# Performance work log

Hardware: AMD Instinct MI355X
Metric: run time of the kernel (lower is better)

The kernel has to match this reference:

```python
import jax, jax.numpy as jnp
import numpy as np

B, S, H, C, LAT = 16, 16, 501, 10, 56
G = H + S  # gate/map input width (mod=None)


def _linear(x, w, b):
    # torch nn.Linear convention: w is [out, in]
    return x @ w.T + b


def _gru_cell(x, h, w_ih, w_hh, b_ih, b_hh):
    gi = _linear(x, w_ih, b_ih)
    gh = _linear(h, w_hh, b_hh)
    i_r, i_z, i_n = jnp.split(gi, 3, axis=-1)
    h_r, h_z, h_n = jnp.split(gh, 3, axis=-1)
    r = jax.nn.sigmoid(i_r + h_r)
    u = jax.nn.sigmoid(i_z + h_z)
    n = jnp.tanh(i_n + r * h_n)
    return (1.0 - u) * n + u * h


def setup_inputs() -> dict:
    key = jax.random.key(0)
    ks = jax.random.split(key, 16)
    w = lambda k, shape: jax.random.normal(k, shape, dtype=jnp.float32) * 0.05
    return {
        "z": jax.random.normal(ks[0], (B, LAT), dtype=jnp.float32),
        "dep_graph": jax.random.uniform(ks[1], (B, S, S), dtype=jnp.float32),
        "node_encoding": jax.random.normal(ks[2], (B, S, C), dtype=jnp.float32),
        "lin1_w": w(ks[3], (H, LAT)), "lin1_b": jnp.zeros((H,), jnp.float32),
        "av1_w": w(ks[4], (2 * H, H)), "av1_b": jnp.zeros((2 * H,), jnp.float32),
        "av2_w": w(ks[5], (C, 2 * H)), "av2_b": jnp.zeros((C,), jnp.float32),
        "ae1_w": w(ks[6], (4 * H, 2 * H)), "ae1_b": jnp.zeros((4 * H,), jnp.float32),
        "ae2_w": w(ks[7], (1, 4 * H)), "ae2_b": jnp.zeros((1,), jnp.float32),
        "gate_w": w(ks[8], (H, G)), "gate_b": jnp.zeros((H,), jnp.float32),
        "map_w": w(ks[9], (H, G)), "map_b": jnp.zeros((H,), jnp.float32),
        "gru_w_ih": w(ks[10], (3 * H, C)), "gru_b_ih": jnp.zeros((3 * H,), jnp.float32),
        "gru_w_hh": w(ks[11], (3 * H, H)), "gru_b_hh": jnp.zeros((3 * H,), jnp.float32),
    }


def reference(z, dep_graph, node_encoding, lin1_w, lin1_b, av1_w, av1_b, av2_w, av2_b,
              ae1_w, ae1_b, ae2_w, ae2_b, gate_w, gate_b, map_w, map_b,
              gru_w_ih, gru_b_ih, gru_w_hh, gru_b_hh):
    Bv, Sv, _ = dep_graph.shape
    Hv = lin1_w.shape[0]
    dt = dep_graph.dtype
    # 'ordering' one-hot positional features, identical per batch element
    ordering = jnp.broadcast_to(jnp.eye(Sv, dtype=dt), (Bv, Sv, Sv))
    col = jnp.arange(Sv)

    add_vertex = lambda x: _linear(jax.nn.relu(_linear(x, av1_w, av1_b)), av2_w, av2_b)
    add_edge = lambda x: _linear(jax.nn.relu(_linear(x, ae1_w, ae1_b)), ae2_w, ae2_b)
    gru = lambda x, h: _gru_cell(x, h, gru_w_ih, gru_w_hh, gru_b_ih, gru_b_hh)

    graph_state = _linear(z, lin1_w, lin1_b)                     # [B, H]
    nhs = jnp.zeros((Bv, Sv, Hv), dt)                            # node hidden states
    gen_dep = jnp.zeros_like(dep_graph)
    gen_nodes = []

    for index in range(Sv):  # static outer loop (seq_len is small & fixed)
        gen_nodes.append(add_vertex(graph_state))                # logits [B, C]
        x_t = node_encoding[:, index]                            # [B, C]
        h0 = graph_state if index == 0 else jnp.zeros((Bv, Hv), dt)
        hv = gru(x_t, h0)
        if index > 0:
            ancestors = dep_graph[:, index]                      # [B, S]

            def inner(carry, v_j):
                hv, nhs = carry
                hidden_j = jnp.take(nhs, v_j, axis=1)            # [B, H]
                edge = add_edge(jnp.concatenate([hv, hidden_j], axis=1))[:, 0]  # [B]
                am = ancestors * (col >= v_j).astype(dt)         # masked ancestors [B, S]
                mhs = jnp.concatenate([nhs, ordering], axis=-1) * am[:, :, None]  # [B,S,H+S]
                h_in = jnp.sum(
                    jax.nn.sigmoid(_linear(mhs, gate_w, gate_b))
                    * _linear(mhs, map_w, map_b)
                    * am[:, :, None],
                    axis=1,
                )                                                # [B, H]
                hv_new = gru(x_t, h_in)
                nhs = nhs.at[:, index].set(hv_new)
                return (hv_new, nhs), edge

            (hv, nhs), edges = jax.lax.scan(inner, (hv, nhs), jnp.arange(index - 1, -1, -1))
            # edges[k] corresponds to v_j = index-1-k -> flip to ascending v_j order
            gen_dep = gen_dep.at[:, index, :index].set(jnp.flip(edges, 0).T)
        nhs = nhs.at[:, index].set(hv)
        graph_state = hv

    gen_node_encoding = jnp.stack(gen_nodes, axis=1)             # [B, S, C]
    return gen_dep, gen_node_encoding
```

## Files before the change

kernel.cpp:

```cpp
#include <hip/hip_runtime.h>

#define DEVFN static __device__ __forceinline__

namespace {
constexpr int Hc = 501, Gc = 517;
constexpr size_t OFF_WGP = 0;
constexpr size_t OFF_WMP = OFF_WGP + (size_t)512 * 512;
constexpr size_t OFF_WHP = OFF_WMP + (size_t)512 * 512;
constexpr size_t OFF_WHV = OFF_WHP + (size_t)512 * 1536;
constexpr size_t OFF_WHJ = OFF_WHV + (size_t)2048 * 512;
constexpr size_t OFF_WAV = OFF_WHJ + (size_t)2048 * 512;
constexpr size_t OFF_GCOL= OFF_WAV + (size_t)1024 * 512;
constexpr size_t OFF_MCOL= OFF_GCOL + (size_t)512 * 16;
constexpr size_t OFF_GI  = OFF_MCOL + (size_t)512 * 16;
constexpr size_t OFF_GS0 = OFF_GI  + (size_t)16 * 16 * 1536;
constexpr size_t OFF_HSEQ= OFF_GS0 + (size_t)16 * 512;
constexpr size_t OFF_HINS= OFF_HSEQ+ (size_t)16 * 136 * 512;
constexpr size_t OFF_TBUF= OFF_HINS+ (size_t)120 * 16 * 512;
constexpr size_t WS_FLOATS=OFF_TBUF+ (size_t)16 * 16 * 1024;
constexpr size_t N_FLG   = (size_t)8 * 256 * 32;
constexpr size_t WS_NEED = (WS_FLOATS + N_FLG + 512 + 64) * 4;

constexpr int SM_WHH = 0;
constexpr int SM_ST  = 24576;
constexpr int SM_QM  = 25600;
constexpr int SM_PS  = 26560;
constexpr int SM_GC  = 27072;
constexpr int SM_GIL = 27584;
constexpr int SM_BHH = 27680;
constexpr int SM_GB  = 27728;
constexpr int SM_MB  = 27744;
constexpr int SM_DEP = 27760;
constexpr int SM_TOT = 27792;
constexpr int F_BHJ = 8192;
constexpr int F_RED = 10112;
constexpr int F_TOT = 10376;
}

DEVFN float sigf(float x)  { return 1.0f / (1.0f + __expf(-x)); }
DEVFN float tanhf_(float x){ float e2 = __expf(2.0f * x); return 1.0f - 2.0f / (e2 + 1.0f); }
DEVFN void  stgf(float* p, float v) { __hip_atomic_store(p, v, __ATOMIC_RELAXED, __HIP_MEMORY_SCOPE_AGENT); }
DEVFN size_t hslotf(int b, int slot) { return OFF_HSEQ + ((size_t)b * 136 + slot) * 512; }
DEVFN int trif(int idx) { return idx * (idx + 1) / 2; }

struct KArgs {
  const float* in[21];
  float* out;
  float* wsf;
};

DEVFN float4 maskpad(float4 v, int k4) {
  if (k4 == 125) { v.y = 0.f; v.z = 0.f; v.w = 0.f; }
  else if (k4 > 125) { v.x = v.y = v.z = v.w = 0.f; }
  return v;
}

__global__ __launch_bounds__(256) void k0_init(KArgs a) {
  const float* z    = a.in[0];  const float* enc  = a.in[2];
  const float* lin1w= a.in[3];  const float* lin1b= a.in[4];
  const float* gatew= a.in[13]; const float* mapw = a.in[15];
  const float* wih  = a.in[17]; const float* bih  = a.in[18];
  const float* whh  = a.in[19];
  float* wsf = a.wsf;
  const int gtid = blockIdx.x * 256 + threadIdx.x;
  const int NTH = 256 * 256;

  for (size_t t = gtid; t < (size_t)512 * 512; t += NTH) {
    int i = t >> 9, k = t & 511;
    bool ok = (i < Hc && k < Hc);
    wsf[OFF_WGP + t] = ok ? gatew[(size_t)i * Gc + k] : 0.f;
    wsf[OFF_WMP + t] = ok ? mapw [(size_t)i * Gc + k] : 0.f;
  }
  for (size_t t = gtid; t < (size_t)512 * 1536; t += NTH) {
    int i = t / 1536, rk = t % 1536, r = rk >> 9, k = rk & 511;
    wsf[OFF_WHP + t] = (i < Hc && k < Hc) ? whh[((size_t)r * Hc + i) * Hc + k] : 0.f;
  }
  for (size_t t = gtid; t < (size_t)512 * 16; t += NTH) {
    int i = t >> 4, j = t & 15;
    wsf[OFF_GCOL + t] = (i < Hc) ? gatew[(size_t)i * Gc + Hc + j] : 0.f;
    wsf[OFF_MCOL + t] = (i < Hc) ? mapw [(size_t)i * Gc + Hc + j] : 0.f;
  }
  for (size_t t = gtid; t < (size_t)16 * 16 * 1503; t += NTH) {
    int r = t % 1503; size_t bi = t / 1503;
    float acc = bih[r];
    const float* x = enc + bi * 10;
    const float* w = wih + (size_t)r * 10;
    #pragma unroll
    for (int c = 0; c < 10; ++c) acc = fmaf(w[c], x[c], acc);
    wsf[OFF_GI + bi * 1536 + r] = acc;
  }
  for (size_t t = gtid; t < (size_t)16 * 512; t += NTH) {
    int b = t >> 9, i = t & 511;
    float v = 0.f;
    if (i < Hc) {
      float acc = lin1b[i];
      const float* zz = z + (size_t)b * 56;
      const float* w  = lin1w + (size_t)i * 56;
      for (int k = 0; k < 56; ++k) acc = fmaf(w[k], zz[k], acc);
      v = acc;
    }
    wsf[OFF_GS0 + t] = v;
  }
  for (size_t t = gtid; t < 4096; t += NTH) a.out[t] = 0.f;
  unsigned* FLG = (unsigned*)a.wsf + WS_FLOATS;
  for (size_t t = gtid; t < N_FLG + 512; t += NTH) FLG[t] = 0u;
}

__global__ __launch_bounds__(256, 1) void k1_scan(KArgs a) {
  const int blk = blockIdx.x, tid = threadIdx.x;
  const int g = blk >> 5, m = blk & 31;
  const int ig = tid >> 4, l = tid & 15;
  const int i = m * 16 + ig;
  float* wsf = a.wsf;
  unsigned* FLG = (unsigned*)a.wsf + WS_FLOATS;
  const float* dep  = a.in[1];
  const float* gateb= a.in[14]; const float* mapb = a.in[16];
  const float* bhh  = a.in[20];

  __shared__ float smem[SM_TOT];
  int pid = 0;

  {
    float4* d = (float4*)smem;
    const float4* s = ((const float4*)(wsf + OFF_WHP)) + (size_t)m * 6144;
    for (int t = tid; t < 6144; t += 256) d[t] = s[t];
    for (int t = tid; t < 512; t += 256) {
      int q = t >> 8, r2 = t & 255, ii = r2 >> 4, j = r2 & 15;
      smem[SM_GC + t] = wsf[(q ? OFF_MCOL : OFF_GCOL) + (size_t)(m * 16 + ii) * 16 + j];
    }
    if (tid < 16) {
      int iG = m * 16 + tid;
      smem[SM_GB + tid] = (iG < Hc) ? gateb[iG] : 0.f;
      smem[SM_MB + tid] = (iG < Hc) ? mapb[iG]  : 0.f;
    }
    if (tid < 48) {
      int r = tid >> 4, ii = tid & 15, iG = m * 16 + ii;
      smem[SM_BHH + tid] = (iG < Hc) ? bhh[r * Hc + iG] : 0.f;
    }
  }
  float4 wgr[8], wmr[8];
  {
    const float4* pg = ((const float4*)(wsf + OFF_WGP)) + (size_t)i * 128;
    const float4* pm = ((const float4*)(wsf + OFF_WMP)) + (size_t)i * 128;
    #pragma unroll
    for (int t = 0; t < 8; ++t) { wgr[t] = pg[t * 16 + l]; wmr[t] = pm[t * 16 + l]; }
  }
  __syncthreads();

  auto flagbar = [&]() {
    __syncthreads();
    if (tid == 0)
      __hip_atomic_store(FLG + ((size_t)g * 256 + pid) * 32 + m, (unsigned)(pid + 1),
                         __ATOMIC_RELAXED, __HIP_MEMORY_SCOPE_AGENT);
    if (tid < 32) {
      unsigned* p = FLG + ((size_t)g * 256 + pid) * 32 + tid;
      while (__hip_atomic_load(p, __ATOMIC_RELAXED, __HIP_MEMORY_SCOPE_AGENT) != (unsigned)(pid + 1))
        __builtin_amdgcn_s_sleep(2);
    }
    __syncthreads();
    ++pid;
  };

  auto stage2v = [&](size_t o0, size_t o1) {
    float4* d = (float4*)(smem + SM_ST);
    if (tid < 128) d[tid] = ((const float4*)(wsf + o0))[tid];
    else           d[tid] = ((const float4*)(wsf + o1))[tid - 128];
  };
  auto stagegi = [&](int index) {
    if (tid >= 64 && tid < 160) {
      int t = tid - 64, b = t / 48, r = (t / 16) % 3, ii = t & 15, iG = m * 16 + ii;
      smem[SM_GIL + (b * 3 + r) * 16 + ii] =
        (iG < Hc) ? wsf[OFF_GI + ((size_t)(2 * g + b) * 16 + index) * 1536 + (size_t)r * Hc + iG] : 0.f;
    }
  };
  auto s1core = [&](float& aq0, float& am0, float& aq1, float& am1) {
    const float4* h0 = (const float4*)(smem + SM_ST);
    const float4* h1 = (const float4*)(smem + SM_ST + 512);
    float q0 = 0.f, m0 = 0.f, q1 = 0.f, m1 = 0.f;
    #pragma unroll
    for (int t = 0; t < 8; ++t) {
      int k4 = t * 16 + l;
      float4 a0 = h0[k4], a1 = h1[k4];
      q0 = fmaf(wgr[t].x, a0.x, q0); q0 = fmaf(wgr[t].y, a0.y, q0);
      q0 = fmaf(wgr[t].z, a0.z, q0); q0 = fmaf(wgr[t].w, a0.w, q0);
      m0 = fmaf(wmr[t].x, a0.x, m0); m0 = fmaf(wmr[t].y, a0.y, m0);
      m0 = fmaf(wmr[t].z, a0.z, m0); m0 = fmaf(wmr[t].w, a0.w, m0);
      q1 = fmaf(wgr[t].x, a1.x, q1); q1 = fmaf(wgr[t].y, a1.y, q1);
      q1 = fmaf(wgr[t].z, a1.z, q1); q1 = fmaf(wgr[t].w, a1.w, q1);
      m1 = fmaf(wmr[t].x, a1.x, m1); m1 = fmaf(wmr[t].y, a1.y, m1);
      m1 = fmaf(wmr[t].z, a1.z, m1); m1 = fmaf(wmr[t].w, a1.w, m1);
    }
    q0 += __shfl_xor(q0, 1); q0 += __shfl_xor(q0, 2); q0 += __shfl_xor(q0, 4); q0 += __shfl_xor(q0, 8);
    m0 += __shfl_xor(m0, 1); m0 += __shfl_xor(m0, 2); m0 += __shfl_xor(m0, 4); m0 += __shfl_xor(m0, 8);
    q1 += __shfl_xor(q1, 1); q1 += __shfl_xor(q1, 2); q1 += __shfl_xor(q1, 4); q1 += __shfl_xor(q1, 8);
    m1 += __shfl_xor(m1, 1); m1 += __shfl_xor(m1, 2); m1 += __shfl_xor(m1, 4); m1 += __shfl_xor(m1, 8);
    aq0 = q0; am0 = m0; aq1 = q1; am1 = m1;
  };
  auto s2core = [&](int dstSlot) {
    const float4* W  = ((const float4*)smem) + ig * 384;
    const float4* h0 = (const float4*)(smem + SM_ST);
    const float4* h1 = (const float4*)(smem + SM_ST + 512);
    float gr0 = 0.f, gz0 = 0.f, gn0 = 0.f, gr1 = 0.f, gz1 = 0.f, gn1 = 0.f;
    #pragma unroll
    for (int t = 0; t < 8; ++t) {
      int k4 = t * 16 + l;
      float4 hv0 = h0[k4], hv1 = h1[k4];
      float4 a0 = W[k4], a1 = W[128 + k4], a2 = W[256 + k4];
      gr0 = fmaf(a0.x, hv0.x, gr0); gr0 = fmaf(a0.y, hv0.y, gr0); gr0 = fmaf(a0.z, hv0.z, gr0); gr0 = fmaf(a0.w, hv0.w, gr0);
      gz0 = fmaf(a1.x, hv0.x, gz0); gz0 = fmaf(a1.y, hv0.y, gz0); gz0 = fmaf(a1.z, hv0.z, gz0); gz0 = fmaf(a1.w, hv0.w, gz0);
      gn0 = fmaf(a2.x, hv0.x, gn0); gn0 = fmaf(a2.y, hv0.y, gn0); gn0 = fmaf(a2.z, hv0.z, gn0); gn0 = fmaf(a2.w, hv0.w, gn0);
      gr1 = fmaf(a0.x, hv1.x, gr1); gr1 = fmaf(a0.y, hv1.y, gr1); gr1 = fmaf(a0.z, hv1.z, gr1); gr1 = fmaf(a0.w, hv1.w, gr1);
      gz1 = fmaf(a1.x, hv1.x, gz1); gz1 = fmaf(a1.y, hv1.y, gz1); gz1 = fmaf(a1.z, hv1.z, gz1); gz1 = fmaf(a1.w, hv1.w, gz1);
      gn1 = fmaf(a2.x, hv1.x, gn1); gn1 = fmaf(a2.y, hv1.y, gn1); gn1 = fmaf(a2.z, hv1.z, gn1); gn1 = fmaf(a2.w, hv1.w, gn1);
    }
    gr0 += __shfl_xor(gr0, 1); gr0 += __shfl_xor(gr0, 2); gr0 += __shfl_xor(gr0, 4); gr0 += __shfl_xor(gr0, 8);
    gz0 += __shfl_xor(gz0, 1); gz0 += __shfl_xor(gz0, 2); gz0 += __shfl_xor(gz0, 4); gz0 += __shfl_xor(gz0, 8);
    gn0 += __shfl_xor(gn0, 1); gn0 += __shfl_xor(gn0, 2); gn0 += __shfl_xor(gn0, 4); gn0 += __shfl_xor(gn0, 8);
    gr1 += __shfl_xor(gr1, 1); gr1 += __shfl_xor(gr1, 2); gr1 += __shfl_xor(gr1, 4); gr1 += __shfl_xor(gr1, 8);
    gz1 += __shfl_xor(gz1, 1); gz1 += __shfl_xor(gz1, 2); gz1 += __shfl_xor(gz1, 4); gz1 += __shfl_xor(gz1, 8);
    gn1 += __shfl_xor(gn1, 1); gn1 += __shfl_xor(gn1, 2); gn1 += __shfl_xor(gn1, 4); gn1 += __shfl_xor(gn1, 8);
    if (l < 2) {
      int b = l;
      float gr = l ? gr1 : gr0, gz = l ? gz1 : gz0, gn = l ? gn1 : gn0;
      float h  = smem[SM_ST + b * 512 + i];
      float rr = sigf(smem[SM_GIL + (b * 3 + 0) * 16 + ig] + gr + smem[SM_BHH + 0 + ig]);
      float uu = sigf(smem[SM_GIL + (b * 3 + 1) * 16 + ig] + gz + smem[SM_BHH + 16 + ig]);
      float nn = tanhf_(smem[SM_GIL + (b * 3 + 2) * 16 + ig] + rr * (gn + smem[SM_BHH + 32 + ig]));
      float v = (1.f - uu) * nn + uu * h;
      if (i >= Hc) v = 0.f;
      stgf(wsf + hslotf(2 * g + b, dstSlot) + i, v);
    }
  };

  stage2v(OFF_GS0 + (size_t)(2 * g) * 512, OFF_GS0 + (size_t)(2 * g + 1) * 512);
  stagegi(0);
  __syncthreads();
  s2core(0);
  flagbar();

  for (int index = 1; index < 16; ++index) {
    stage2v(hslotf(2 * g,     trif(index - 1) + index - 1),
            hslotf(2 * g + 1, trif(index - 1) + index - 1));
    if (tid < 32) {
      int b = tid >> 4, j = tid & 15;
      smem[SM_DEP + b * 16 + j] = dep[((size_t)(2 * g + b) * 16 + index) * 16 + j];
    }
    stagegi(index);
    __syncthreads();
    {
      float aq0, am0, aq1, am1;
      s1core(aq0, am0, aq1, am1);
      if (l < 2) {
        float aq = l ? aq1 : aq0, am = l ? am1 : am0;
        smem[SM_QM + ((l * 2 + 0) * 15 + (index - 1)) * 16 + ig] = aq + smem[SM_GC + ig * 16 + (index - 1)];
        smem[SM_QM + ((l * 2 + 1) * 15 + (index - 1)) * 16 + ig] = am + smem[SM_GC + 256 + ig * 16 + (index - 1)];
      }
    }
    __syncthreads();
    if (l < 2) {
      float acc = 0.f, gb = smem[SM_GB + ig], mb = smem[SM_MB + ig];
      for (int j = 15; j >= 0; --j) {
        if (j != index) {
          float aa = smem[SM_DEP + l * 16 + j];
          float q, mm;
          if (j < index) { q = smem[SM_QM + ((l * 2 + 0) * 15 + j) * 16 + ig];
                           mm = smem[SM_QM + ((l * 2 + 1) * 15 + j) * 16 + ig]; }
          else           { q = smem[SM_GC + ig * 16 + j];
                           mm = smem[SM_GC + 256 + ig * 16 + j]; }
          float sg = sigf(fmaf(aa, q, gb));
          acc = fmaf(aa * sg, fmaf(aa, mm, mb), acc);
        }
        smem[SM_PS + (l * 16 + ig) * 16 + j] = acc;
      }
    } else if (l < 4) {
      int b = l - 2;
      float rr = sigf(smem[SM_GIL + (b * 3 + 0) * 16 + ig] + smem[SM_BHH + 0 + ig]);
      float uu = sigf(smem[SM_GIL + (b * 3 + 1) * 16 + ig] + smem[SM_BHH + 16 + ig]);
      float nn = tanhf_(smem[SM_GIL + (b * 3 + 2) * 16 + ig] + rr * smem[SM_BHH + 32 + ig]);
      float v = (1.f - uu) * nn;
      if (i >= Hc) v = 0.f;
      stgf(wsf + hslotf(2 * g + b, trif(index) + 0) + i, v);
    }
    __syncthreads();
    if (l < 2) {
      int b = l;
      float gb = smem[SM_GB + ig], mb = smem[SM_MB + ig];
      float aI = smem[SM_DEP + b * 16 + index];
      float Qi = smem[SM_GC + ig * 16 + index], Mi = smem[SM_GC + 256 + ig * 16 + index];
      float f = aI * sigf(fmaf(aI, Qi, gb)) * fmaf(aI, Mi, mb);
      float v = smem[SM_PS + (b * 16 + ig) * 16 + (index - 1)] + f;
      if (i >= Hc) v = 0.f;
      stgf(wsf + OFF_HINS + ((size_t)(index * (index - 1) / 2 + 0) * 16 + (2 * g + b)) * 512 + i, v);
    }
    flagbar();

    for (int s = 0; s < index; ++s) {
      stage2v(OFF_HINS + ((size_t)(index * (index - 1) / 2 + s) * 16 + (2 * g + 0)) * 512,
              OFF_HINS + ((size_t)(index * (index - 1) / 2 + s) * 16 + (2 * g + 1)) * 512);
      __syncthreads();
      s2core(trif(index) + s + 1);
      flagbar();
      if (s + 1 < index) {
        int ss = s + 1, vj = index - 1 - ss;
        stage2v(hslotf(2 * g, trif(index) + ss), hslotf(2 * g + 1, trif(index) + ss));
        __syncthreads();
        {
          float aq0, am0, aq1, am1;
          s1core(aq0, am0, aq1, am1);
          if (l < 2) {
            int b = l;
            float aq = l ? aq1 : aq0, am = l ? am1 : am0;
            float gb = smem[SM_GB + ig], mb = smem[SM_MB + ig];
            float aI = smem[SM_DEP + b * 16 + index];
            float Qi = aq + smem[SM_GC + ig * 16 + index];
            float Mi = am + smem[SM_GC + 256 + ig * 16 + index];
            float f = aI * sigf(fmaf(aI, Qi, gb)) * fmaf(aI, Mi, mb);
            float v = smem[SM_PS + (b * 16 + ig) * 16 + vj] + f;
            if (i >= Hc) v = 0.f;
            stgf(wsf + OFF_HINS + ((size_t)(index * (index - 1) / 2 + ss) * 16 + (2 * g + b)) * 512 + i, v);
          }
        }
        flagbar();
      }
    }
  }
}

__global__ __launch_bounds__(256, 1) void k2_fin(KArgs a) {
  const int blk = blockIdx.x, tid = threadIdx.x;
  float* wsf = a.wsf;
  unsigned* FLG = (unsigned*)a.wsf + WS_FLOATS;
  unsigned* F1F = FLG + N_FLG;
  const float* ae1w = a.in[9];
  const float* av1w = a.in[5];

  __shared__ float smem[F_TOT];
  const int b = blk >> 4, rs = blk & 15;
  const int il = tid >> 3, l8 = tid & 7;
  float4* lds4 = (float4*)smem;

  for (int t = tid; t < 2048; t += 256) {
    int j = t >> 7, k4 = t & 127;
    float4 v = {0.f, 0.f, 0.f, 0.f};
    if (j < 15) v = maskpad(((const float4*)(wsf + hslotf(b, trif(j) + j)))[k4], k4);
    lds4[t] = v;
  }
  __syncthreads();
  {
    const int rbase = rs * 126 + il * 4;
    for (int half = 0; half < 2; ++half) {
      int jbase = half * 8;
      float acc[4][8];
      #pragma unroll
      for (int q = 0; q < 4; ++q)
        #pragma unroll
        for (int j = 0; j < 8; ++j) acc[q][j] = 0.f;
      for (int s = 0; s < 63; ++s) {
        int k = s * 8 + l8;
        if (k < 501) {
          float w[4];
          #pragma unroll
          for (int q = 0; q < 4; ++q)
            w[q] = (rbase + q < 2004) ? ae1w[(size_t)(rbase + q) * 1002 + 501 + k] : 0.f;
          float hv[8];
          #pragma unroll
          for (int j = 0; j < 8; ++j) hv[j] = smem[(jbase + j) * 512 + k];
          #pragma unroll
          for (int q = 0; q < 4; ++q)
            #pragma unroll
            for (int j = 0; j < 8; ++j) acc[q][j] = fmaf(w[q], hv[j], acc[q][j]);
        }
      }
      #pragma unroll
      for (int q = 0; q < 4; ++q) {
        bool rowok = (il * 4 + q < 126) && (rbase + q < 2004);
        #pragma unroll
        for (int j = 0; j < 8; ++j) {
          float v = acc[q][j];
          v += __shfl_xor(v, 1); v += __shfl_xor(v, 2); v += __shfl_xor(v, 4);
          if (l8 == 0 && rowok && (jbase + j) < 15)
            smem[F_BHJ + (jbase + j) * 128 + il * 4 + q] = v;
        }
      }
    }
  }
  __syncthreads();
  for (int t = tid; t < 2048; t += 256) {
    int idx = t >> 7, k4 = t & 127;
    const float4* src = (idx == 0)
      ? ((const float4*)(wsf + OFF_GS0 + (size_t)b * 512))
      : ((const float4*)(wsf + hslotf(b, trif(idx - 1) + idx - 1)));
    lds4[t] = maskpad(src[k4], k4);
  }
  __syncthreads();
  {
    const float* av1b = a.in[6];
    const int rbase = rs * 63 + il * 2;
    for (int half = 0; half < 2; ++half) {
      int jbase = half * 8;
      float acc[2][8];
      #pragma unroll
      for (int q = 0; q < 2; ++q)
        #pragma unroll
        for (int j = 0; j < 8; ++j) acc[q][j] = 0.f;
      for (int s = 0; s < 63; ++s) {
        int k = s * 8 + l8;
        if (k < 501) {
          float w[2];
          #pragma unroll
          for (int q = 0; q < 2; ++q)
            w[q] = (rbase + q < 1002) ? av1w[(size_t)(rbase + q) * 501 + k] : 0.f;
          float hv[8];
          #pragma unroll
          for (int j = 0; j < 8; ++j) hv[j] = smem[(jbase + j) * 512 + k];
          #pragma unroll
          for (int q = 0; q < 2; ++q)
            #pragma unroll
            for (int j = 0; j < 8; ++j) acc[q][j] = fmaf(w[q], hv[j], acc[q][j]);
        }
      }
      #pragma unroll
      for (int q = 0; q < 2; ++q) {
        int r = rbase + q;
        bool rowok = (il * 2 + q < 63) && (r < 1002);
        float b1 = rowok ? av1b[r] : 0.f;
        #pragma unroll
        for (int j = 0; j < 8; ++j) {
          float v = acc[q][j];
          v += __shfl_xor(v, 1); v += __shfl_xor(v, 2); v += __shfl_xor(v, 4);
          if (l8 == 0 && rowok)
            stgf(wsf + OFF_TBUF + ((size_t)b * 16 + jbase + j) * 1024 + r, fmaxf(v + b1, 0.f));
        }
      }
    }
  }
  __syncthreads();
  if (tid == 0)
    __hip_atomic_store(F1F + b * 16 + rs, 1u, __ATOMIC_RELAXED, __HIP_MEMORY_SCOPE_AGENT);

  const float* ae1b = a.in[10]; const float* ae2w = a.in[11]; const float* ae2b = a.in[12];
  const int rbase = rs * 126 + il * 4;
  for (int chunk = 0; chunk < 15; ++chunk) {
    int idxs[8], vjs[8]; bool tval[8];
    #pragma unroll
    for (int j = 0; j < 8; ++j) {
      int e = chunk * 8 + j;
      if (e < 120) {
        int ix = 1, rem = e;
        while (rem >= ix) { rem -= ix; ++ix; }
        idxs[j] = ix; vjs[j] = rem; tval[j] = true;
      } else { idxs[j] = 1; vjs[j] = 0; tval[j] = false; }
    }
    __syncthreads();
    for (int t = tid; t < 1024; t += 256) {
      int sl = t >> 7, k4 = t & 127;
      int sE = idxs[sl] - 1 - vjs[sl];
      lds4[t] = maskpad(((const float4*)(wsf + hslotf(b, trif(idxs[sl]) + sE)))[k4], k4);
    }
    __syncthreads();
    float part[8];
    #pragma unroll
    for (int j = 0; j < 8; ++j) part[j] = 0.f;
    float acc[4][8];
    #pragma unroll
    for (int q = 0; q < 4; ++q)
      #pragma unroll
      for (int j = 0; j < 8; ++j) acc[q][j] = 0.f;
    for (int s = 0; s < 63; ++s) {
      int k = s * 8 + l8;
      if (k < 501) {
        float w[4];
        #pragma unroll
        for (int q = 0; q < 4; ++q)
          w[q] = (rbase + q < 2004) ? ae1w[(size_t)(rbase + q) * 1002 + k] : 0.f;
        float hv[8];
        #pragma unroll
        for (int j = 0; j < 8; ++j) hv[j] = smem[j * 512 + k];
        #pragma unroll
        for (int q = 0; q < 4; ++q)
          #pragma unroll
          for (int j = 0; j < 8; ++j) acc[q][j] = fmaf(w[q], hv[j], acc[q][j]);
      }
    }
    #pragma unroll
    for (int q = 0; q < 4; ++q) {
      int r = rbase + q;
      bool rowok = (il * 4 + q < 126) && (r < 2004);
      float aer = rowok ? ae2w[r] : 0.f;
      float b1r = rowok ? ae1b[r] : 0.f;
      #pragma unroll
      for (int j = 0; j < 8; ++j) {
        float v = acc[q][j];
        v += __shfl_xor(v, 1); v += __shfl_xor(v, 2); v += __shfl_xor(v, 4);
        if (l8 == 0 && rowok && tval[j]) {
          float bh = smem[F_BHJ + vjs[j] * 128 + il * 4 + q];
          part[j] = fmaf(aer, fmaxf(v + bh + b1r, 0.f), part[j]);
        }
      }
    }
    if (l8 == 0) {
      #pragma unroll
      for (int j = 0; j < 8; ++j) smem[F_RED + il * 8 + j] = part[j];
    }
    __syncthreads();
    if (tid < 8) {
      float v = 0.f;
      for (int q = 0; q < 32; ++q) v += smem[F_RED + q * 8 + tid];
      if (rs == 0) v += ae2b[0];
      if (tval[tid])
        atomicAdd(a.out + ((size_t)b * 16 + idxs[tid]) * 16 + vjs[tid], v);
    }
    __syncthreads();
  }
  if (tid < 16) {
    unsigned* p = F1F + b * 16 + tid;
    while (__hip_atomic_load(p, __ATOMIC_RELAXED, __HIP_MEMORY_SCOPE_AGENT) != 1u)
      __builtin_amdgcn_s_sleep(2);
  }
  __syncthreads();
  {
    const float* av2w = a.in[7]; const float* av2b = a.in[8];
    const float* tb = wsf + OFF_TBUF + ((size_t)b * 16 + rs) * 1024;
    float accn[10];
    #pragma unroll
    for (int c = 0; c < 10; ++c) accn[c] = 0.f;
    for (int r = tid; r < 1002; r += 256) {
      float tv = tb[r];
      #pragma unroll
      for (int c = 0; c < 10; ++c) accn[c] = fmaf(av2w[(size_t)c * 1002 + r], tv, accn[c]);
    }
    #pragma unroll
    for (int c = 0; c < 10; ++c) {
      float v = accn[c];
      for (int m2 = 1; m2 < 64; m2 <<= 1) v += __shfl_xor(v, m2);
      if ((tid & 63) == 0) smem[F_RED + (tid >> 6) * 10 + c] = v;
    }
    __syncthreads();
    if (tid == 0) {
      for (int c = 0; c < 10; ++c) {
        float v = av2b[c] + smem[F_RED + c] + smem[F_RED + 10 + c] + smem[F_RED + 20 + c] + smem[F_RED + 30 + c];
        stgf(a.out + 4096 + ((size_t)b * 16 + rs) * 10 + c, v);
      }
    }
  }
}

extern "C" void kernel_launch(void* const* d_in, const int* in_sizes, int n_in,
                              void* d_out, int out_size, void* d_ws, size_t ws_size,
                              hipStream_t stream) {
  (void)in_sizes; (void)n_in; (void)out_size;
  if (ws_size < WS_NEED) return;
  KArgs a;
  for (int k = 0; k < 21; ++k) a.in[k] = (const float*)d_in[k];
  a.out = (float*)d_out;
  a.wsf = (float*)d_ws;
  k0_init<<<256, 256, 0, stream>>>(a);
  k1_scan<<<256, 256, 0, stream>>>(a);
  k2_fin <<<256, 256, 0, stream>>>(a);
}
```

Measured before the change: 1.330 ms.

## Replace flag barriers with NaN-sentinel data polling in scan kernel

Removes the per-step cross-block flag barrier and instead pre-fills the hidden-state and h_in buffers with NaN sentinels. Each block polls the specific data it needs until the values are no longer NaN, turning the global barrier into fine-grained dataflow synchronization. This cuts the barrier round trips and lets blocks proceed as soon as their inputs arrive. The risks are correctness: it relies on non-NaN data, on write visibility without acquire ordering, and on float4 pieces not being torn. It also adds init work to fill the buffers.

```diff
diff --git a/kernel.cpp b/kernel.cpp
--- a/kernel.cpp
+++ b/kernel.cpp
@@ -101,9 +101,14 @@
     }
     wsf[OFF_GS0 + t] = v;
   }
+  {
+    unsigned* p = (unsigned*)(wsf + OFF_HSEQ);
+    const size_t n = OFF_TBUF - OFF_HSEQ;
+    for (size_t t = gtid; t < n; t += NTH) p[t] = 0x7FC00000u;
+  }
   for (size_t t = gtid; t < 4096; t += NTH) a.out[t] = 0.f;
   unsigned* FLG = (unsigned*)a.wsf + WS_FLOATS;
-  for (size_t t = gtid; t < N_FLG + 512; t += NTH) FLG[t] = 0u;
+  for (size_t t = gtid; t < 512; t += NTH) FLG[N_FLG + t] = 0u;
 }
 
 __global__ __launch_bounds__(256, 1) void k1_scan(KArgs a) {
@@ -112,13 +117,11 @@
   const int ig = tid >> 4, l = tid & 15;
   const int i = m * 16 + ig;
   float* wsf = a.wsf;
-  unsigned* FLG = (unsigned*)a.wsf + WS_FLOATS;
   const float* dep  = a.in[1];
   const float* gateb= a.in[14]; const float* mapb = a.in[16];
   const float* bhh  = a.in[20];
 
   __shared__ float smem[SM_TOT];
-  int pid = 0;
 
   {
     float4* d = (float4*)smem;
@@ -145,26 +148,19 @@
     #pragma unroll
     for (int t = 0; t < 8; ++t) { wgr[t] = pg[t * 16 + l]; wmr[t] = pm[t * 16 + l]; }
   }
-  __syncthreads();
-
-  auto flagbar = [&]() {
-    __syncthreads();
-    if (tid == 0)
-      __hip_atomic_store(FLG + ((size_t)g * 256 + pid) * 32 + m, (unsigned)(pid + 1),
-                         __ATOMIC_RELAXED, __HIP_MEMORY_SCOPE_AGENT);
-    if (tid < 32) {
-      unsigned* p = FLG + ((size_t)g * 256 + pid) * 32 + tid;
-      while (__hip_atomic_load(p, __ATOMIC_RELAXED, __HIP_MEMORY_SCOPE_AGENT) != (unsigned)(pid + 1))
-        __builtin_amdgcn_s_sleep(2);
-    }
-    __syncthreads();
-    ++pid;
-  };
-
-  auto stage2v = [&](size_t o0, size_t o1) {
-    float4* d = (float4*)(smem + SM_ST);
-    if (tid < 128) d[tid] = ((const float4*)(wsf + o0))[tid];
-    else           d[tid] = ((const float4*)(wsf + o1))[tid - 128];
+
+  auto pollst = [&](size_t o0, size_t o1) {
+    size_t base = (tid < 128) ? o0 : o1;
+    int idx = (tid & 127) * 4;
+    const volatile float* s = (const volatile float*)(wsf + base) + idx;
+    float x, y, zv, w;
+    for (;;) {
+      x = s[0]; y = s[1]; zv = s[2]; w = s[3];
+      if (!(x != x || y != y || zv != zv || w != w)) break;
+      __builtin_amdgcn_s_sleep(1);
+    }
+    float* d = smem + SM_ST + (tid < 128 ? 0 : 512) + idx;
+    d[0] = x; d[1] = y; d[2] = zv; d[3] = w;
   };
   auto stagegi = [&](int index) {
     if (tid >= 64 && tid < 160) {
@@ -232,15 +228,16 @@
     }
   };
 
-  stage2v(OFF_GS0 + (size_t)(2 * g) * 512, OFF_GS0 + (size_t)(2 * g + 1) * 512);
+  __syncthreads();
+  pollst(OFF_GS0 + (size_t)(2 * g) * 512, OFF_GS0 + (size_t)(2 * g + 1) * 512);
   stagegi(0);
   __syncthreads();
   s2core(0);
-  flagbar();
 
   for (int index = 1; index < 16; ++index) {
-    stage2v(hslotf(2 * g,     trif(index - 1) + index - 1),
-            hslotf(2 * g + 1, trif(index - 1) + index - 1));
+    __syncthreads();
+    pollst(hslotf(2 * g,     trif(index - 1) + index - 1),
+           hslotf(2 * g + 1, trif(index - 1) + index - 1));
     if (tid < 32) {
       int b = tid >> 4, j = tid & 15;
       smem[SM_DEP + b * 16 + j] = dep[((size_t)(2 * g + b) * 16 + index) * 16 + j];
@@ -292,17 +289,17 @@
       if (i >= Hc) v = 0.f;
       stgf(wsf + OFF_HINS + ((size_t)(index * (index - 1) / 2 + 0) * 16 + (2 * g + b)) * 512 + i, v);
     }
-    flagbar();
 
     for (int s = 0; s < index; ++s) {
-      stage2v(OFF_HINS + ((size_t)(index * (index - 1) / 2 + s) * 16 + (2 * g + 0)) * 512,
-              OFF_HINS + ((size_t)(index * (index - 1) / 2 + s) * 16 + (2 * g + 1)) * 512);
+      __syncthreads();
+      pollst(OFF_HINS + ((size_t)(index * (index - 1) / 2 + s) * 16 + (2 * g + 0)) * 512,
+             OFF_HINS + ((size_t)(index * (index - 1) / 2 + s) * 16 + (2 * g + 1)) * 512);
       __syncthreads();
       s2core(trif(index) + s + 1);
-      flagbar();
       if (s + 1 < index) {
         int ss = s + 1, vj = index - 1 - ss;
-        stage2v(hslotf(2 * g, trif(index) + ss), hslotf(2 * g + 1, trif(index) + ss));
+        __syncthreads();
+        pollst(hslotf(2 * g, trif(index) + ss), hslotf(2 * g + 1, trif(index) + ss));
         __syncthreads();
         {
           float aq0, am0, aq1, am1;
@@ -320,7 +317,6 @@
             stgf(wsf + OFF_HINS + ((size_t)(index * (index - 1) / 2 + ss) * 16 + (2 * g + b)) * 512 + i, v);
           }
         }
-        flagbar();
       }
     }
   }
```

After: 1.370 ms. 1.03x slower.

## Move weight repacking and GI precompute into scan kernel; prefetch edge-MLP inputs

Applied to the files above, without the earlier changes.

The scan kernel now reads gate, map and GRU weights straight from the raw inputs into shared memory and registers, and computes the input-gate projections and initial state locally. This removes the large repack pass in the init kernel and its workspace round-trip, and the init kernel shrinks to 64 blocks. The final kernel register-prefetches the next chunk of hidden states into a double-buffered LDS region and prefetches the av1 input tile. Bounds checks in its inner loops are replaced by clamped indices. Strided non-vectorised weight loads in the scan kernel's prologue may cost more per block.

```diff
diff --git a/kernel.cpp b/kernel.cpp
--- a/kernel.cpp
+++ b/kernel.cpp
@@ -4,16 +4,7 @@
 
 namespace {
 constexpr int Hc = 501, Gc = 517;
-constexpr size_t OFF_WGP = 0;
-constexpr size_t OFF_WMP = OFF_WGP + (size_t)512 * 512;
-constexpr size_t OFF_WHP = OFF_WMP + (size_t)512 * 512;
-constexpr size_t OFF_WHV = OFF_WHP + (size_t)512 * 1536;
-constexpr size_t OFF_WHJ = OFF_WHV + (size_t)2048 * 512;
-constexpr size_t OFF_WAV = OFF_WHJ + (size_t)2048 * 512;
-constexpr size_t OFF_GCOL= OFF_WAV + (size_t)1024 * 512;
-constexpr size_t OFF_MCOL= OFF_GCOL + (size_t)512 * 16;
-constexpr size_t OFF_GI  = OFF_MCOL + (size_t)512 * 16;
-constexpr size_t OFF_GS0 = OFF_GI  + (size_t)16 * 16 * 1536;
+constexpr size_t OFF_GS0 = (size_t)7 * 1024 * 1024;
 constexpr size_t OFF_HSEQ= OFF_GS0 + (size_t)16 * 512;
 constexpr size_t OFF_HINS= OFF_HSEQ+ (size_t)16 * 136 * 512;
 constexpr size_t OFF_TBUF= OFF_HINS+ (size_t)120 * 16 * 512;
@@ -26,12 +17,12 @@
 constexpr int SM_QM  = 25600;
 constexpr int SM_PS  = 26560;
 constexpr int SM_GC  = 27072;
-constexpr int SM_GIL = 27584;
-constexpr int SM_BHH = 27680;
-constexpr int SM_GB  = 27728;
-constexpr int SM_MB  = 27744;
-constexpr int SM_DEP = 27760;
-constexpr int SM_TOT = 27792;
+constexpr int SM_GIS = 27584;
+constexpr int SM_BHH = 29120;
+constexpr int SM_GB  = 29168;
+constexpr int SM_MB  = 29184;
+constexpr int SM_DEP = 29200;
+constexpr int SM_TOT = 29232;
 constexpr int F_BHJ = 8192;
 constexpr int F_RED = 10112;
 constexpr int F_TOT = 10376;
@@ -42,6 +33,7 @@
 DEVFN void  stgf(float* p, float v) { __hip_atomic_store(p, v, __ATOMIC_RELAXED, __HIP_MEMORY_SCOPE_AGENT); }
 DEVFN size_t hslotf(int b, int slot) { return OFF_HSEQ + ((size_t)b * 136 + slot) * 512; }
 DEVFN int trif(int idx) { return idx * (idx + 1) / 2; }
+DEVFN int mini(int a, int b) { return a < b ? a : b; }
 
 struct KArgs {
   const float* in[21];
@@ -56,51 +48,8 @@
 }
 
 __global__ __launch_bounds__(256) void k0_init(KArgs a) {
-  const float* z    = a.in[0];  const float* enc  = a.in[2];
-  const float* lin1w= a.in[3];  const float* lin1b= a.in[4];
-  const float* gatew= a.in[13]; const float* mapw = a.in[15];
-  const float* wih  = a.in[17]; const float* bih  = a.in[18];
-  const float* whh  = a.in[19];
-  float* wsf = a.wsf;
   const int gtid = blockIdx.x * 256 + threadIdx.x;
-  const int NTH = 256 * 256;
-
-  for (size_t t = gtid; t < (size_t)512 * 512; t += NTH) {
-    int i = t >> 9, k = t & 511;
-    bool ok = (i < Hc && k < Hc);
-    wsf[OFF_WGP + t] = ok ? gatew[(size_t)i * Gc + k] : 0.f;
-    wsf[OFF_WMP + t] = ok ? mapw [(size_t)i * Gc + k] : 0.f;
-  }
-  for (size_t t = gtid; t < (size_t)512 * 1536; t += NTH) {
-    int i = t / 1536, rk = t % 1536, r = rk >> 9, k = rk & 511;
-    wsf[OFF_WHP + t] = (i < Hc && k < Hc) ? whh[((size_t)r * Hc + i) * Hc + k] : 0.f;
-  }
-  for (size_t t = gtid; t < (size_t)512 * 16; t += NTH) {
-    int i = t >> 4, j = t & 15;
-    wsf[OFF_GCOL + t] = (i < Hc) ? gatew[(size_t)i * Gc + Hc + j] : 0.f;
-    wsf[OFF_MCOL + t] = (i < Hc) ? mapw [(size_t)i * Gc + Hc + j] : 0.f;
-  }
-  for (size_t t = gtid; t < (size_t)16 * 16 * 1503; t += NTH) {
-    int r = t % 1503; size_t bi = t / 1503;
-    float acc = bih[r];
-    const float* x = enc + bi * 10;
-    const float* w = wih + (size_t)r * 10;
-    #pragma unroll
-    for (int c = 0; c < 10; ++c) acc = fmaf(w[c], x[c], acc);
-    wsf[OFF_GI + bi * 1536 + r] = acc;
-  }
-  for (size_t t = gtid; t < (size_t)16 * 512; t += NTH) {
-    int b = t >> 9, i = t & 511;
-    float v = 0.f;
-    if (i < Hc) {
-      float acc = lin1b[i];
-      const float* zz = z + (size_t)b * 56;
-      const float* w  = lin1w + (size_t)i * 56;
-      for (int k = 0; k < 56; ++k) acc = fmaf(w[k], zz[k], acc);
-      v = acc;
-    }
-    wsf[OFF_GS0 + t] = v;
-  }
+  const int NTH = 64 * 256;
   for (size_t t = gtid; t < 4096; t += NTH) a.out[t] = 0.f;
   unsigned* FLG = (unsigned*)a.wsf + WS_FLOATS;
   for (size_t t = gtid; t < N_FLG + 512; t += NTH) FLG[t] = 0u;
@@ -113,37 +62,78 @@
   const int i = m * 16 + ig;
   float* wsf = a.wsf;
   unsigned* FLG = (unsigned*)a.wsf + WS_FLOATS;
-  const float* dep  = a.in[1];
-  const float* gateb= a.in[14]; const float* mapb = a.in[16];
-  const float* bhh  = a.in[20];
+  const float* z    = a.in[0];  const float* dep  = a.in[1];  const float* enc = a.in[2];
+  const float* lin1w= a.in[3];  const float* lin1b= a.in[4];
+  const float* gatew= a.in[13]; const float* gateb= a.in[14];
+  const float* mapw = a.in[15]; const float* mapb = a.in[16];
+  const float* wih  = a.in[17]; const float* bih  = a.in[18];
+  const float* whh  = a.in[19]; const float* bhh  = a.in[20];
 
   __shared__ float smem[SM_TOT];
   int pid = 0;
 
-  {
-    float4* d = (float4*)smem;
-    const float4* s = ((const float4*)(wsf + OFF_WHP)) + (size_t)m * 6144;
-    for (int t = tid; t < 6144; t += 256) d[t] = s[t];
-    for (int t = tid; t < 512; t += 256) {
-      int q = t >> 8, r2 = t & 255, ii = r2 >> 4, j = r2 & 15;
-      smem[SM_GC + t] = wsf[(q ? OFF_MCOL : OFF_GCOL) + (size_t)(m * 16 + ii) * 16 + j];
-    }
-    if (tid < 16) {
-      int iG = m * 16 + tid;
-      smem[SM_GB + tid] = (iG < Hc) ? gateb[iG] : 0.f;
-      smem[SM_MB + tid] = (iG < Hc) ? mapb[iG]  : 0.f;
-    }
-    if (tid < 48) {
-      int r = tid >> 4, ii = tid & 15, iG = m * 16 + ii;
-      smem[SM_BHH + tid] = (iG < Hc) ? bhh[r * Hc + iG] : 0.f;
-    }
+  for (int t = tid; t < 16 * 1536; t += 256) {
+    int ig2 = t / 1536, rk = t % 1536, r = rk >> 9, k = rk & 511;
+    int i2 = m * 16 + ig2;
+    smem[t] = (i2 < Hc && k < Hc) ? whh[((size_t)(r * Hc + i2)) * Hc + k] : 0.f;
+  }
+  for (int t = tid; t < 512; t += 256) {
+    int q = t >> 8, r2 = t & 255, ii = r2 >> 4, j = r2 & 15;
+    int iG = m * 16 + ii;
+    const float* W = q ? mapw : gatew;
+    smem[SM_GC + t] = (iG < Hc) ? W[(size_t)iG * Gc + Hc + j] : 0.f;
+  }
+  for (int t = tid; t < 1536; t += 256) {
+    int ig3 = t & 15, u = t >> 4, r = u % 3, v2 = u / 3, idx = v2 & 15, b = v2 >> 4;
+    int iG = m * 16 + ig3;
+    float val = 0.f;
+    if (iG < Hc) {
+      int rr = r * Hc + iG;
+      const float* x = enc + ((size_t)(2 * g + b) * 16 + idx) * 10;
+      float acc = bih[rr];
+      const float* w = wih + (size_t)rr * 10;
+      #pragma unroll
+      for (int c = 0; c < 10; ++c) acc = fmaf(w[c], x[c], acc);
+      val = acc;
+    }
+    smem[SM_GIS + t] = val;
+  }
+  if (tid < 16) {
+    int iG = m * 16 + tid;
+    smem[SM_GB + tid] = (iG < Hc) ? gateb[iG] : 0.f;
+    smem[SM_MB + tid] = (iG < Hc) ? mapb[iG]  : 0.f;
+  }
+  if (tid >= 64 && tid < 112) {
+    int t = tid - 64, r = t >> 4, ii = t & 15, iG = m * 16 + ii;
+    smem[SM_BHH + t] = (iG < Hc) ? bhh[r * Hc + iG] : 0.f;
   }
   float4 wgr[8], wmr[8];
-  {
-    const float4* pg = ((const float4*)(wsf + OFF_WGP)) + (size_t)i * 128;
-    const float4* pm = ((const float4*)(wsf + OFF_WMP)) + (size_t)i * 128;
-    #pragma unroll
-    for (int t = 0; t < 8; ++t) { wgr[t] = pg[t * 16 + l]; wmr[t] = pm[t * 16 + l]; }
+  #pragma unroll
+  for (int t = 0; t < 8; ++t) {
+    int kb = (t * 16 + l) * 4;
+    float gv[4], mv[4];
+    #pragma unroll
+    for (int c = 0; c < 4; ++c) {
+      int kk = kb + c;
+      bool ok = (i < Hc && kk < Hc);
+      gv[c] = ok ? gatew[(size_t)i * Gc + kk] : 0.f;
+      mv[c] = ok ? mapw [(size_t)i * Gc + kk] : 0.f;
+    }
+    wgr[t] = make_float4(gv[0], gv[1], gv[2], gv[3]);
+    wmr[t] = make_float4(mv[0], mv[1], mv[2], mv[3]);
+  }
+  for (int t = tid; t < 1024; t += 256) {
+    int b = t >> 9, ii = t & 511;
+    float v = 0.f;
+    if (ii < Hc) {
+      float acc = lin1b[ii];
+      const float* zz = z + (size_t)(2 * g + b) * 56;
+      const float* w  = lin1w + (size_t)ii * 56;
+      for (int k = 0; k < 56; ++k) acc = fmaf(w[k], zz[k], acc);
+      v = acc;
+    }
+    smem[SM_ST + t] = v;
+    if (m == 0) stgf(wsf + OFF_GS0 + (size_t)2 * g * 512 + t, v);
   }
   __syncthreads();
 
@@ -165,13 +155,6 @@
     float4* d = (float4*)(smem + SM_ST);
     if (tid < 128) d[tid] = ((const float4*)(wsf + o0))[tid];
     else           d[tid] = ((const float4*)(wsf + o1))[tid - 128];
-  };
-  auto stagegi = [&](int index) {
-    if (tid >= 64 && tid < 160) {
-      int t = tid - 64, b = t / 48, r = (t / 16) % 3, ii = t & 15, iG = m * 16 + ii;
-      smem[SM_GIL + (b * 3 + r) * 16 + ii] =
-        (iG < Hc) ? wsf[OFF_GI + ((size_t)(2 * g + b) * 16 + index) * 1536 + (size_t)r * Hc + iG] : 0.f;
-    }
   };
   auto s1core = [&](float& aq0, float& am0, float& aq1, float& am1) {
     const float4* h0 = (const float4*)(smem + SM_ST);
@@ -196,7 +179,7 @@
     m1 += __shfl_xor(m1, 1); m1 += __shfl_xor(m1, 2); m1 += __shfl_xor(m1, 4); m1 += __shfl_xor(m1, 8);
     aq0 = q0; am0 = m0; aq1 = q1; am1 = m1;
   };
-  auto s2core = [&](int dstSlot) {
+  auto s2core = [&](int index, int dstSlot) {
     const float4* W  = ((const float4*)smem) + ig * 384;
     const float4* h0 = (const float4*)(smem + SM_ST);
     const float4* h1 = (const float4*)(smem + SM_ST + 512);
@@ -223,19 +206,17 @@
       int b = l;
       float gr = l ? gr1 : gr0, gz = l ? gz1 : gz0, gn = l ? gn1 : gn0;
       float h  = smem[SM_ST + b * 512 + i];
-      float rr = sigf(smem[SM_GIL + (b * 3 + 0) * 16 + ig] + gr + smem[SM_BHH + 0 + ig]);
-      float uu = sigf(smem[SM_GIL + (b * 3 + 1) * 16 + ig] + gz + smem[SM_BHH + 16 + ig]);
-      float nn = tanhf_(smem[SM_GIL + (b * 3 + 2) * 16 + ig] + rr * (gn + smem[SM_BHH + 32 + ig]));
+      const int gb2 = SM_GIS + ((b * 16 + index) * 3) * 16 + ig;
+      float rr = sigf(smem[gb2 + 0]  + gr + smem[SM_BHH + 0 + ig]);
+      float uu = sigf(smem[gb2 + 16] + gz + smem[SM_BHH + 16 + ig]);
+      float nn = tanhf_(smem[gb2 + 32] + rr * (gn + smem[SM_BHH + 32 + ig]));
       float v = (1.f - uu) * nn + uu * h;
       if (i >= Hc) v = 0.f;
       stgf(wsf + hslotf(2 * g + b, dstSlot) + i, v);
     }
   };
 
-  stage2v(OFF_GS0 + (size_t)(2 * g) * 512, OFF_GS0 + (size_t)(2 * g + 1) * 512);
-  stagegi(0);
-  __syncthreads();
-  s2core(0);
+  s2core(0, 0);
   flagbar();
 
   for (int index = 1; index < 16; ++index) {
@@ -245,7 +226,6 @@
       int b = tid >> 4, j = tid & 15;
       smem[SM_DEP + b * 16 + j] = dep[((size_t)(2 * g + b) * 16 + index) * 16 + j];
     }
-    stagegi(index);
     __syncthreads();
     {
       float aq0, am0, aq1, am1;
@@ -274,9 +254,10 @@
       }
     } else if (l < 4) {
       int b = l - 2;
-      float rr = sigf(smem[SM_GIL + (b * 3 + 0) * 16 + ig] + smem[SM_BHH + 0 + ig]);
-      float uu = sigf(smem[SM_GIL + (b * 3 + 1) * 16 + ig] + smem[SM_BHH + 16 + ig]);
-      float nn = tanhf_(smem[SM_GIL + (b * 3 + 2) * 16 + ig] + rr * smem[SM_BHH + 32 + ig]);
+      const int gb2 = SM_GIS + ((b * 16 + index) * 3) * 16 + ig;
+      float rr = sigf(smem[gb2 + 0]  + smem[SM_BHH + 0 + ig]);
+      float uu = sigf(smem[gb2 + 16] + smem[SM_BHH + 16 + ig]);
+      float nn = tanhf_(smem[gb2 + 32] + rr * smem[SM_BHH + 32 + ig]);
       float v = (1.f - uu) * nn;
       if (i >= Hc) v = 0.f;
       stgf(wsf + hslotf(2 * g + b, trif(index) + 0) + i, v);
@@ -298,7 +279,7 @@
       stage2v(OFF_HINS + ((size_t)(index * (index - 1) / 2 + s) * 16 + (2 * g + 0)) * 512,
               OFF_HINS + ((size_t)(index * (index - 1) / 2 + s) * 16 + (2 * g + 1)) * 512);
       __syncthreads();
-      s2core(trif(index) + s + 1);
+      s2core(index, trif(index) + s + 1);
       flagbar();
       if (s + 1 < index) {
         int ss = s + 1, vj = index - 1 - ss;
@@ -346,8 +327,20 @@
     lds4[t] = v;
   }
   __syncthreads();
+  float4 pfb[8];
+  #pragma unroll
+  for (int p = 0; p < 8; ++p) {
+    int fidx = p * 256 + tid, idx = fidx >> 7, k4 = fidx & 127;
+    const float4* src = (idx == 0)
+      ? ((const float4*)(wsf + OFF_GS0 + (size_t)b * 512))
+      : ((const float4*)(wsf + hslotf(b, trif(idx - 1) + idx - 1)));
+    pfb[p] = maskpad(src[k4], k4);
+  }
   {
     const int rbase = rs * 126 + il * 4;
+    int rq[4];
+    #pragma unroll
+    for (int q = 0; q < 4; ++q) rq[q] = mini(rbase + q, 2003);
     for (int half = 0; half < 2; ++half) {
       int jbase = half * 8;
       float acc[4][8];
@@ -357,19 +350,17 @@
         for (int j = 0; j < 8; ++j) acc[q][j] = 0.f;
       for (int s = 0; s < 63; ++s) {
         int k = s * 8 + l8;
-        if (k < 501) {
-          float w[4];
+        int kc = (k > 500) ? 500 : k;
+        float w[4];
+        #pragma unroll
+        for (int q = 0; q < 4; ++q) w[q] = ae1w[(size_t)rq[q] * 1002 + 501 + kc];
+        float hv[8];
+        #pragma unroll
+        for (int j = 0; j < 8; ++j) hv[j] = smem[(jbase + j) * 512 + k];
+        #pragma unroll
+        for (int q = 0; q < 4; ++q)
           #pragma unroll
-          for (int q = 0; q < 4; ++q)
-            w[q] = (rbase + q < 2004) ? ae1w[(size_t)(rbase + q) * 1002 + 501 + k] : 0.f;
-          float hv[8];
-          #pragma unroll
-          for (int j = 0; j < 8; ++j) hv[j] = smem[(jbase + j) * 512 + k];
-          #pragma unroll
-          for (int q = 0; q < 4; ++q)
-            #pragma unroll
-            for (int j = 0; j < 8; ++j) acc[q][j] = fmaf(w[q], hv[j], acc[q][j]);
-        }
+          for (int j = 0; j < 8; ++j) acc[q][j] = fmaf(w[q], hv[j], acc[q][j]);
       }
       #pragma unroll
       for (int q = 0; q < 4; ++q) {
@@ -385,17 +376,15 @@
     }
   }
   __syncthreads();
-  for (int t = tid; t < 2048; t += 256) {
-    int idx = t >> 7, k4 = t & 127;
-    const float4* src = (idx == 0)
-      ? ((const float4*)(wsf + OFF_GS0 + (size_t)b * 512))
-      : ((const float4*)(wsf + hslotf(b, trif(idx - 1) + idx - 1)));
-    lds4[t] = maskpad(src[k4], k4);
-  }
+  #pragma unroll
+  for (int p = 0; p < 8; ++p) lds4[p * 256 + tid] = pfb[p];
   __syncthreads();
   {
     const float* av1b = a.in[6];
     const int rbase = rs * 63 + il * 2;
+    int rq[2];
+    #pragma unroll
+    for (int q = 0; q < 2; ++q) rq[q] = mini(rbase + q, 1001);
     for (int half = 0; half < 2; ++half) {
       int jbase = half * 8;
       float acc[2][8];
@@ -405,19 +394,17 @@
         for (int j = 0; j < 8; ++j) acc[q][j] = 0.f;
       for (int s = 0; s < 63; ++s) {
         int k = s * 8 + l8;
-        if (k < 501) {
-          float w[2];
+        int kc = (k > 500) ? 500 : k;
+        float w[2];
+        #pragma unroll
+        for (int q = 0; q < 2; ++q) w[q] = av1w[(size_t)rq[q] * 501 + kc];
+        float hv[8];
+        #pragma unroll
+        for (int j = 0; j < 8; ++j) hv[j] = smem[(jbase + j) * 512 + k];
+        #pragma unroll
+        for (int q = 0; q < 2; ++q)
           #pragma unroll
-          for (int q = 0; q < 2; ++q)
-            w[q] = (rbase + q < 1002) ? av1w[(size_t)(rbase + q) * 501 + k] : 0.f;
-          float hv[8];
-          #pragma unroll
-          for (int j = 0; j < 8; ++j) hv[j] = smem[(jbase + j) * 512 + k];
-          #pragma unroll
-          for (int q = 0; q < 2; ++q)
-            #pragma unroll
-            for (int j = 0; j < 8; ++j) acc[q][j] = fmaf(w[q], hv[j], acc[q][j]);
-        }
+          for (int j = 0; j < 8; ++j) acc[q][j] = fmaf(w[q], hv[j], acc[q][j]);
       }
       #pragma unroll
       for (int q = 0; q < 2; ++q) {
@@ -440,8 +427,10 @@
 
   const float* ae1b = a.in[10]; const float* ae2w = a.in[11]; const float* ae2b = a.in[12];
   const int rbase = rs * 126 + il * 4;
-  for (int chunk = 0; chunk < 15; ++chunk) {
-    int idxs[8], vjs[8]; bool tval[8];
+  int rq[4];
+  #pragma unroll
+  for (int q = 0; q < 4; ++q) rq[q] = mini(rbase + q, 2003);
+  auto decode = [&](int chunk, int* idxs, int* vjs, bool* tval) {
     #pragma unroll
     for (int j = 0; j < 8; ++j) {
       int e = chunk * 8 + j;
@@ -451,16 +440,33 @@
         idxs[j] = ix; vjs[j] = rem; tval[j] = true;
       } else { idxs[j] = 1; vjs[j] = 0; tval[j] = false; }
     }
-    __syncthreads();
+  };
+  {
+    int idxs[8], vjs[8]; bool tval[8];
+    decode(0, idxs, vjs, tval);
     for (int t = tid; t < 1024; t += 256) {
       int sl = t >> 7, k4 = t & 127;
       int sE = idxs[sl] - 1 - vjs[sl];
       lds4[t] = maskpad(((const float4*)(wsf + hslotf(b, trif(idxs[sl]) + sE)))[k4], k4);
     }
-    __syncthreads();
-    float part[8];
-    #pragma unroll
-    for (int j = 0; j < 8; ++j) part[j] = 0.f;
+  }
+  __syncthreads();
+  int cur = 0;
+  for (int chunk = 0; chunk < 15; ++chunk) {
+    int idxs[8], vjs[8]; bool tval[8];
+    decode(chunk, idxs, vjs, tval);
+    float4 pf[4];
+    if (chunk < 14) {
+      int nidxs[8], nvjs[8]; bool ntval[8];
+      decode(chunk + 1, nidxs, nvjs, ntval);
+      #pragma unroll
+      for (int p = 0; p < 4; ++p) {
+        int fidx = p * 256 + tid, sl = fidx >> 7, k4 = fidx & 127;
+        int sE = nidxs[sl] - 1 - nvjs[sl];
+        pf[p] = maskpad(((const float4*)(wsf + hslotf(b, trif(nidxs[sl]) + sE)))[k4], k4);
+      }
+    }
+    const float* hbuf = smem + cur * 4096;
     float acc[4][8];
     #pragma unroll
     for (int q = 0; q < 4; ++q)
@@ -468,20 +474,21 @@
       for (int j = 0; j < 8; ++j) acc[q][j] = 0.f;
     for (int s = 0; s < 63; ++s) {
       int k = s * 8 + l8;
-      if (k < 501) {
-        float w[4];
-        #pragma unroll
-        for (int q = 0; q < 4; ++q)
-          w[q] = (rbase + q < 2004) ? ae1w[(size_t)(rbase + q) * 1002 + k] : 0.f;
-        float hv[8];
-        #pragma unroll
-        for (int j = 0; j < 8; ++j) hv[j] = smem[j * 512 + k];
-        #pragma unroll
-        for (int q = 0; q < 4; ++q)
-          #pragma unroll
-          for (int j = 0; j < 8; ++j) acc[q][j] = fmaf(w[q], hv[j], acc[q][j]);
-      }
-    }
+      int kc = (k > 500) ? 500 : k;
+      float w[4];
+      #pragma unroll
+      for (int q = 0; q < 4; ++q) w[q] = ae1w[(size_t)rq[q] * 1002 + kc];
+      float hv[8];
+      #pragma unroll
+      for (int j = 0; j < 8; ++j) hv[j] = hbuf[j * 512 + k];
+      #pragma unroll
+      for (int q = 0; q < 4; ++q)
+        #pragma unroll
+        for (int j = 0; j < 8; ++j) acc[q][j] = fmaf(w[q], hv[j], acc[q][j]);
+    }
+    float part[8];
+    #pragma unroll
+    for (int j = 0; j < 8; ++j) part[j] = 0.f;
     #pragma unroll
     for (int q = 0; q < 4; ++q) {
       int r = rbase + q;
@@ -511,6 +518,12 @@
         atomicAdd(a.out + ((size_t)b * 16 + idxs[tid]) * 16 + vjs[tid], v);
     }
     __syncthreads();
+    if (chunk < 14) {
+      #pragma unroll
+      for (int p = 0; p < 4; ++p) lds4[(1 - cur) * 1024 + p * 256 + tid] = pf[p];
+      cur = 1 - cur;
+      __syncthreads();
+    }
   }
   if (tid < 16) {
     unsigned* p = F1F + b * 16 + tid;
@@ -554,7 +567,7 @@
   for (int k = 0; k < 21; ++k) a.in[k] = (const float*)d_in[k];
   a.out = (float*)d_out;
   a.wsf = (float*)d_ws;
-  k0_init<<<256, 256, 0, stream>>>(a);
+  k0_init<<<64, 256, 0, stream>>>(a);
   k1_scan<<<256, 256, 0, stream>>>(a);
   k2_fin <<<256, 256, 0, stream>>>(a);
 }
```

Result: faster. 1.138 ms (-14.4%).
